# Optimization experiments

Measured on AMD Instinct MI355X. Metric: run time of the kernel, lower is better.

Reference implementation:

```python
import jax, jax.numpy as jnp
import numpy as np

# Loihi neuron / simulation constants (params['neuron'], params['simulation'])
VTH_MANT = 80
V_DECAY = 128
I_DECAY = 1024
REF_DELAY = 1
WGT_EXP = 0
TAU_RHO = 1.0
SCALE_RHO = 1.0
TS = 1
THETA = float(VTH_MANT * (1 << 6))      # 5120, Loihi threshold in fixed-point units
W_SCALE = float(1 << (6 + WGT_EXP))     # 64, weight scaling into Loihi fixed point


def st_floor(x):
    """floor with straight-through gradient (Loihi integer truncation)."""
    return x + jax.lax.stop_gradient(jnp.floor(x) - x)


@jax.custom_vjp
def spike_fn(v):
    # binary spike scaled by 1/Ts, as in SLAYER-Loihi
    return (v >= THETA).astype(v.dtype) * (1.0 / TS)

def _spike_fwd(v):
    return spike_fn(v), v

def _spike_bwd(v, g):
    # SLAYER surrogate: scaleRho/(tauRho*theta) * exp(-|v - theta| / (tauRho*theta))
    pdf = (SCALE_RHO / (TAU_RHO * THETA)) * jnp.exp(-jnp.abs(v - THETA) / (TAU_RHO * THETA))
    return (g * pdf,)

spike_fn.defvjp(_spike_fwd, _spike_bwd)


def quantize_w(w, step=2.0):
    """SLAYER snn.utils.quantize(w, 2) with straight-through gradient."""
    return w + jax.lax.stop_gradient(jnp.round(w / step) * step - w)


def loihi_spikes(wsp):
    """Loihi CUBA neuron scan. wsp: [T, B, C] weighted spike input -> [T, B, C] spikes."""
    i_mul = (4096.0 - I_DECAY) / 4096.0
    v_mul = (4096.0 - V_DECAY) / 4096.0

    def step(carry, x):
        I, V, ref = carry
        I = st_floor(I * i_mul) + W_SCALE * x
        V = st_floor(V * v_mul) + I
        V = jnp.where(ref > 0, jnp.zeros_like(V), V)   # refractory hold at 0
        s = spike_fn(V)
        V = V * (1.0 - s * TS)                          # reset to 0 on spike
        ref = jnp.where(s > 0, REF_DELAY - 1, jnp.maximum(ref - 1, 0))
        return (I, V, ref), s

    B, C = wsp.shape[1], wsp.shape[2]
    init = (jnp.zeros((B, C), wsp.dtype),
            jnp.zeros((B, C), wsp.dtype),
            jnp.zeros((B, C), jnp.int32))
    _, s = jax.lax.scan(step, init, wsp)
    return s


def delay_shift(x):
    """delayShift(x, 1): shift spikes one step forward in time. x: [T, B, C]."""
    return jnp.concatenate([jnp.zeros_like(x[:1]), x[:-1]], axis=0)


def setup_inputs() -> dict:
    key = jax.random.key(0)
    k1, k2, k3 = jax.random.split(key, 3)
    B, IN, HID, OUT, T = 32, 1024, 2048, 512, 256
    spike_input = (jax.random.uniform(k1, (B, IN, T)) < 0.05).astype(jnp.float32)
    W1 = jax.random.normal(k2, (HID, IN), jnp.float32) * 8.0
    W2 = jax.random.normal(k3, (OUT, HID), jnp.float32) * 8.0
    return {"spike_input": spike_input, "W1": W1, "W2": W2}


def reference(spike_input, W1, W2):
    # spike_input: [B, IN, T] binary spikes
    x = jnp.transpose(spike_input, (2, 0, 1))          # [T, B, IN]
    w1 = quantize_w(W1)
    w2 = quantize_w(W2)
    h = jnp.einsum('tbi,hi->tbh', x, w1)               # fc1 per timestep
    s1 = delay_shift(loihi_spikes(h))                  # spikeLoihi + delayShift(1)
    o = jnp.einsum('tbh,oh->tbo', s1, w2)              # fc2 per timestep
    s2 = delay_shift(loihi_spikes(o))
    return jnp.transpose(s2, (1, 2, 0))                # [B, OUT, T]
```

## Files before the change

kernel.cpp:

```cpp
#include <hip/hip_runtime.h>

typedef unsigned char u8;
typedef signed char i8;
typedef unsigned int u32;
typedef __attribute__((ext_vector_type(4))) int i32x4;

#define AS1 __attribute__((address_space(1)))
#define AS3 __attribute__((address_space(3)))

__device__ __forceinline__ void gload_lds16(const void* g, void* l) {
    __builtin_amdgcn_global_load_lds((const AS1 void*)g, (AS3 void*)l, 16, 0, 0);
}

__global__ void transpose_x_bt(const float* __restrict__ X, i8* __restrict__ Xb,
                               int B, int IN, int T) {
    __shared__ float tile[128][33];
    const int t0 = blockIdx.x * 32, i0 = blockIdx.y * 128, b = blockIdx.z;
    const int tx = threadIdx.x & 31, ty = threadIdx.x >> 5;
    const float* src = X + (size_t)b * IN * T;
#pragma unroll
    for (int r = 0; r < 16; ++r) {
        int i = ty + r * 8;
        tile[i][tx] = src[(size_t)(i0 + i) * T + t0 + tx];
    }
    __syncthreads();
    const int cx = threadIdx.x & 31;
    const int tl0 = threadIdx.x >> 5;
#pragma unroll
    for (int r = 0; r < 4; ++r) {
        int tl = tl0 + r * 8;
        uchar4 pk;
        pk.x = (tile[cx * 4 + 0][tl] != 0.f) ? 1 : 0;
        pk.y = (tile[cx * 4 + 1][tl] != 0.f) ? 1 : 0;
        pk.z = (tile[cx * 4 + 2][tl] != 0.f) ? 1 : 0;
        pk.w = (tile[cx * 4 + 3][tl] != 0.f) ? 1 : 0;
        *(uchar4*)&Xb[((size_t)b * T + t0 + tl) * IN + i0 + cx * 4] = pk;
    }
}

__global__ void quant_both(const float4* __restrict__ W1, const float4* __restrict__ W2,
                           char4* __restrict__ W1q, char4* __restrict__ W2q,
                           int n1v, int n2v) {
    int i = blockIdx.x * 256 + threadIdx.x;
    if (i < n1v) {
        float4 w = W1[i];
        char4 q;
        q.x = (i8)(int)rintf(w.x * 0.5f);
        q.y = (i8)(int)rintf(w.y * 0.5f);
        q.z = (i8)(int)rintf(w.z * 0.5f);
        q.w = (i8)(int)rintf(w.w * 0.5f);
        W1q[i] = q;
    } else if (i < n1v + n2v) {
        int j = i - n1v;
        float4 w = W2[j];
        char4 q;
        q.x = (i8)(int)rintf(w.x * 0.5f);
        q.y = (i8)(int)rintf(w.y * 0.5f);
        q.z = (i8)(int)rintf(w.z * 0.5f);
        q.w = (i8)(int)rintf(w.w * 0.5f);
        W2q[j] = q;
    }
}

__global__ __launch_bounds__(256, 4) void gemm1_scan1(
        const i8* __restrict__ A, const i8* __restrict__ Bt,
        i8* __restrict__ S1, int K) {
    __shared__ __align__(16) i8 lds[40960];
    i8*    lA   = lds;
    i8*    lB   = lds + 32768;
    short* hT   = (short*)lds;
    u32*   bits = (u32*)(lds + 32768);

    const int nwg = gridDim.x;
    const int cpx = nwg >> 3;
    const int wg  = (blockIdx.x & 7) * cpx + (blockIdx.x >> 3);
    const int scanw = (blockIdx.x >> 3) & 3;
    const int bx = wg & 31;
    const int by = wg >> 5;
    const int n0 = bx * 64;
    const int m0 = by * 256;

    const int tid  = threadIdx.x;
    const int lane = tid & 63;
    const int w    = tid >> 6;
    const int l15 = lane & 15;
    const int l4  = lane >> 4;
    const int sw  = l15 & 7;

    i32x4 acc[4][4] = {};
    const int flatT = tid * 16;

    for (int k0 = 0; k0 < K; k0 += 128) {
        __syncthreads();
#pragma unroll
        for (int q = 0; q < 8; ++q) {
            int fl = q * 4096 + flatT;
            int r  = fl >> 7;
            int sc = ((fl >> 4) & 7) ^ (r & 7);
            gload_lds16(A + (size_t)(m0 + r) * K + k0 + sc * 16, &lA[fl]);
        }
#pragma unroll
        for (int q = 0; q < 2; ++q) {
            int fl = q * 4096 + flatT;
            int r  = fl >> 7;
            int sc = ((fl >> 4) & 7) ^ (r & 7);
            gload_lds16(Bt + (size_t)(n0 + r) * K + k0 + sc * 16, &lB[fl]);
        }
        __syncthreads();
#pragma unroll
        for (int kk = 0; kk < 2; ++kk) {
            i32x4 af[4], bf[4];
#pragma unroll
            for (int mf = 0; mf < 4; ++mf)
                af[mf] = *(const i32x4*)&lA[(w * 64 + mf * 16 + l15) * 128 +
                                            ((kk * 4 + l4) ^ sw) * 16];
#pragma unroll
            for (int nf = 0; nf < 4; ++nf)
                bf[nf] = *(const i32x4*)&lB[(nf * 16 + l15) * 128 +
                                            ((kk * 4 + l4) ^ sw) * 16];
#pragma unroll
            for (int mf = 0; mf < 4; ++mf)
#pragma unroll
                for (int nf = 0; nf < 4; ++nf)
                    acc[mf][nf] = __builtin_amdgcn_mfma_i32_16x16x64_i8(
                        af[mf], bf[nf], acc[mf][nf], 0, 0, 0);
        }
    }
    __syncthreads();

#pragma unroll
    for (int mf = 0; mf < 4; ++mf)
#pragma unroll
        for (int nf = 0; nf < 4; ++nf) {
            int n = nf * 16 + l15;
            int c = w * 16 + mf * 4 + l4;
            int h0 = acc[mf][nf][0] * 2, h1 = acc[mf][nf][1] * 2;
            int h2 = acc[mf][nf][2] * 2, h3 = acc[mf][nf][3] * 2;
            int2 pk;
            pk.x = (h0 & 0xffff) | (h1 << 16);
            pk.y = (h2 & 0xffff) | (h3 << 16);
            *(int2*)((char*)hT + n * 512 + ((c ^ (n & 15)) << 3)) = pk;
        }
    __syncthreads();

    if (w == scanw) {
        const int n = lane;
        const int nx = n & 15;
        const char* hrow = (char*)hT + n * 512;
        int2 ra[4], rb[4];
#pragma unroll
        for (int q = 0; q < 4; ++q)
            ra[q] = *(const int2*)(hrow + ((q ^ nx) << 3));
        u32 bw[8] = {0, 0, 0, 0, 0, 0, 0, 0};
        float I = 0.f, V = 0.f;
#pragma unroll
        for (int p = 0; p < 16; ++p) {
            if (p < 15) {
#pragma unroll
                for (int q = 0; q < 4; ++q) {
                    int2 v = *(const int2*)(hrow + ((((p + 1) * 4 + q) ^ nx) << 3));
                    if (p & 1) ra[q] = v; else rb[q] = v;
                }
            }
#pragma unroll
            for (int q = 0; q < 4; ++q) {
                int2 hh = (p & 1) ? rb[q] : ra[q];
#pragma unroll
                for (int j = 0; j < 4; ++j) {
                    int t = p * 16 + q * 4 + j;
                    short hv = (j == 0) ? (short)hh.x
                             : (j == 1) ? (short)(hh.x >> 16)
                             : (j == 2) ? (short)hh.y
                                        : (short)(hh.y >> 16);
                    I = floorf(I * 0.75f) + 64.f * (float)hv;
                    V = floorf(V * 0.96875f) + I;
                    if (V >= 5120.f) { bw[t >> 5] |= (1u << (t & 31)); V = 0.f; }
                }
            }
        }
#pragma unroll
        for (int wi = 0; wi < 8; ++wi) bits[wi * 64 + n] = bw[wi];
    }
    __syncthreads();

#pragma unroll
    for (int rep = 0; rep < 16; ++rep) {
        int d   = rep * 256 + tid;
        int tt  = d >> 4;
        int ndq = d & 15;
        u32 outw = 0;
        if (tt > 0) {
            int tb = tt - 1, wi = tb >> 5, sh = tb & 31;
            outw =  ((bits[wi * 64 + ndq * 4 + 0] >> sh) & 1)
                 | (((bits[wi * 64 + ndq * 4 + 1] >> sh) & 1) << 8)
                 | (((bits[wi * 64 + ndq * 4 + 2] >> sh) & 1) << 16)
                 | (((bits[wi * 64 + ndq * 4 + 3] >> sh) & 1) << 24);
        }
        *(u32*)&S1[(size_t)(m0 + tt) * 2048 + n0 + ndq * 4] = outw;
    }
}

__global__ __launch_bounds__(1024, 1) void gemm2_scan2(
        const i8* __restrict__ A, const i8* __restrict__ Bt,
        float* __restrict__ out, int K) {
    __shared__ __align__(16) i8 lds[83968];
    float* hT   = (float*)lds;
    u32*   bits = (u32*)(lds + 81920);

    const int nwg = gridDim.x;
    const int cpx = nwg >> 3;
    const int wg  = (blockIdx.x & 7) * cpx + (blockIdx.x >> 3);
    const int scanw = (blockIdx.x >> 3) & 15;
    const int ox = wg & 7;
    const int by = wg >> 3;
    const int n0 = ox * 64;
    const int m0 = by * 256;

    const int tid  = threadIdx.x;
    const int lane = tid & 63;
    const int w    = tid >> 6;
    const int l15 = lane & 15;
    const int l4  = lane >> 4;
    const int sw  = l15 & 7;

    i32x4 acc[4] = {};
    const int flatT = tid * 16;

    auto STAGE = [&](int buf, int k0) {
        i8* lA = lds + buf * 40960;
        i8* lB = lA + 32768;
#pragma unroll
        for (int q = 0; q < 2; ++q) {
            int fl = q * 16384 + flatT;
            int r  = fl >> 7;
            int sc = ((fl >> 4) & 7) ^ (r & 7);
            gload_lds16(A + (size_t)(m0 + r) * K + k0 + sc * 16, &lA[fl]);
        }
        if (tid < 512) {
            int fl = flatT;
            int r  = fl >> 7;
            int sc = ((fl >> 4) & 7) ^ (r & 7);
            gload_lds16(Bt + (size_t)(n0 + r) * K + k0 + sc * 16, &lB[fl]);
        }
    };

    auto COMPUTE = [&](int buf) {
        const i8* lA = lds + buf * 40960;
        const i8* lB = lA + 32768;
#pragma unroll
        for (int kk = 0; kk < 2; ++kk) {
            i32x4 af, bf[4];
            af = *(const i32x4*)&lA[(w * 16 + l15) * 128 + ((kk * 4 + l4) ^ sw) * 16];
#pragma unroll
            for (int nf = 0; nf < 4; ++nf)
                bf[nf] = *(const i32x4*)&lB[(nf * 16 + l15) * 128 +
                                            ((kk * 4 + l4) ^ sw) * 16];
#pragma unroll
            for (int nf = 0; nf < 4; ++nf)
                acc[nf] = __builtin_amdgcn_mfma_i32_16x16x64_i8(
                    af, bf[nf], acc[nf], 0, 0, 0);
        }
    };

    STAGE(0, 0);
    __syncthreads();
    int cur = 0;
    for (int k0 = 0; k0 < K; k0 += 128) {
        if (k0 + 128 < K) STAGE(cur ^ 1, k0 + 128);
        COMPUTE(cur);
        __syncthreads();
        cur ^= 1;
    }

#pragma unroll
    for (int nf = 0; nf < 4; ++nf) {
        int n = nf * 16 + l15;
        int c = w * 4 + l4;
        float4 pk;
        pk.x = (float)(acc[nf][0] * 2);
        pk.y = (float)(acc[nf][1] * 2);
        pk.z = (float)(acc[nf][2] * 2);
        pk.w = (float)(acc[nf][3] * 2);
        *(float4*)((char*)hT + n * 1024 + ((c ^ (n & 15)) << 4)) = pk;
    }
    __syncthreads();

    if (w == scanw) {
        const int n = lane;
        const int nx = n & 15;
        const char* hrow = (char*)hT + n * 1024;
        float4 ra[4], rb[4];
#pragma unroll
        for (int q = 0; q < 4; ++q)
            ra[q] = *(const float4*)(hrow + ((q ^ nx) << 4));
        u32 bw[8] = {0, 0, 0, 0, 0, 0, 0, 0};
        float I = 0.f, V = 0.f;
#pragma unroll
        for (int p = 0; p < 16; ++p) {
            if (p < 15) {
#pragma unroll
                for (int q = 0; q < 4; ++q) {
                    float4 v = *(const float4*)(hrow + ((((p + 1) * 4 + q) ^ nx) << 4));
                    if (p & 1) ra[q] = v; else rb[q] = v;
                }
            }
#pragma unroll
            for (int q = 0; q < 4; ++q) {
                float4 hh = (p & 1) ? rb[q] : ra[q];
#pragma unroll
                for (int j = 0; j < 4; ++j) {
                    int t = p * 16 + q * 4 + j;
                    float hv = (j == 0) ? hh.x : (j == 1) ? hh.y
                             : (j == 2) ? hh.z : hh.w;
                    I = floorf(I * 0.75f) + 64.f * hv;
                    V = floorf(V * 0.96875f) + I;
                    if (V >= 5120.f) { bw[t >> 5] |= (1u << (t & 31)); V = 0.f; }
                }
            }
        }
#pragma unroll
        for (int wi = 0; wi < 8; ++wi) bits[wi * 64 + n] = bw[wi];
    }
    __syncthreads();

#pragma unroll
    for (int rep = 0; rep < 4; ++rep) {
        int flat = rep * 1024 + tid;
        int o  = flat >> 6;
        int t4 = flat & 63;
        float4 v;
#pragma unroll
        for (int j = 0; j < 4; ++j) {
            int tt = t4 * 4 + j;
            float s = 0.f;
            if (tt > 0) {
                int tb = tt - 1;
                s = (float)((bits[(tb >> 5) * 64 + o] >> (tb & 31)) & 1);
            }
            if (j == 0) v.x = s; else if (j == 1) v.y = s;
            else if (j == 2) v.z = s; else v.w = s;
        }
        *(float4*)&out[((size_t)by * 512 + n0 + o) * 256 + t4 * 4] = v;
    }
}

extern "C" void kernel_launch(void* const* d_in, const int* in_sizes, int n_in,
                              void* d_out, int out_size, void* d_ws, size_t ws_size,
                              hipStream_t stream) {
    const int B = 32, IN = 1024, HID = 2048, OUT = 512, T = 256;
    const float* spikes = (const float*)d_in[0];
    const float* W1 = (const float*)d_in[1];
    const float* W2 = (const float*)d_in[2];
    float* out = (float*)d_out;

    char* ws = (char*)d_ws;
    size_t off = 0;
    auto alloc = [&](size_t bytes) -> void* {
        void* p = ws + off;
        off += (bytes + 255) & ~(size_t)255;
        return p;
    };
    i8* Xb  = (i8*)alloc((size_t)B * T * IN);
    i8* W1q = (i8*)alloc((size_t)HID * IN);
    i8* W2q = (i8*)alloc((size_t)OUT * HID);
    i8* S1  = (i8*)alloc((size_t)B * T * HID);

    transpose_x_bt<<<dim3(T / 32, IN / 128, B), dim3(256), 0, stream>>>(spikes, Xb, B, IN, T);
    {
        int n1v = HID * IN / 4, n2v = OUT * HID / 4;
        quant_both<<<dim3((n1v + n2v + 255) / 256), dim3(256), 0, stream>>>(
            (const float4*)W1, (const float4*)W2, (char4*)W1q, (char4*)W2q, n1v, n2v);
    }
    gemm1_scan1<<<dim3(1024), dim3(256), 0, stream>>>(Xb, W1q, S1, IN);
    gemm2_scan2<<<dim3(256), dim3(1024), 0, stream>>>(S1, W2q, out, HID);
}
```

Measured before the change: 68.13 us.

## Double-buffer gemm1 LDS staging with K-step 64 and adjusted swizzle

Rewrites the gemm1_scan1 main loop as a two-stage LDS double buffer: the next K=64 slice is fetched with global_load_lds into the alternate buffer while MFMAs run on the current one. This removes one barrier per iteration and lets global loads overlap with compute. The K tile shrinks from 128 to 64, so the XOR swizzle is changed to fit 64-byte rows. The trade-off is twice as many loop iterations, each with fewer MFMAs to hide load latency, plus a new bank-conflict pattern from the narrower rows.

```diff
diff --git a/kernel.cpp b/kernel.cpp
--- a/kernel.cpp
+++ b/kernel.cpp
@@ -66,8 +66,6 @@
         const i8* __restrict__ A, const i8* __restrict__ Bt,
         i8* __restrict__ S1, int K) {
     __shared__ __align__(16) i8 lds[40960];
-    i8*    lA   = lds;
-    i8*    lB   = lds + 32768;
     short* hT   = (short*)lds;
     u32*   bits = (u32*)(lds + 32768);
 
@@ -85,48 +83,57 @@
     const int w    = tid >> 6;
     const int l15 = lane & 15;
     const int l4  = lane >> 4;
-    const int sw  = l15 & 7;
+    const int sw  = (l15 >> 1) & 3;
 
     i32x4 acc[4][4] = {};
     const int flatT = tid * 16;
 
-    for (int k0 = 0; k0 < K; k0 += 128) {
+    auto STAGE = [&](int buf, int k0) {
+        i8* lA = lds + buf * 20480;
+        i8* lB = lA + 16384;
+#pragma unroll
+        for (int q = 0; q < 4; ++q) {
+            int fl = q * 4096 + flatT;
+            int r  = fl >> 6;
+            int sc = ((fl >> 4) & 3) ^ ((r >> 1) & 3);
+            gload_lds16(A + (size_t)(m0 + r) * K + k0 + sc * 16, &lA[fl]);
+        }
+        {
+            int fl = flatT;
+            int r  = fl >> 6;
+            int sc = ((fl >> 4) & 3) ^ ((r >> 1) & 3);
+            gload_lds16(Bt + (size_t)(n0 + r) * K + k0 + sc * 16, &lB[fl]);
+        }
+    };
+
+    auto COMPUTE = [&](int buf) {
+        const i8* lA = lds + buf * 20480;
+        const i8* lB = lA + 16384;
+        i32x4 af[4], bf[4];
+#pragma unroll
+        for (int mf = 0; mf < 4; ++mf)
+            af[mf] = *(const i32x4*)&lA[(w * 64 + mf * 16 + l15) * 64 +
+                                        ((l4 ^ sw) << 4)];
+#pragma unroll
+        for (int nf = 0; nf < 4; ++nf)
+            bf[nf] = *(const i32x4*)&lB[(nf * 16 + l15) * 64 + ((l4 ^ sw) << 4)];
+#pragma unroll
+        for (int mf = 0; mf < 4; ++mf)
+#pragma unroll
+            for (int nf = 0; nf < 4; ++nf)
+                acc[mf][nf] = __builtin_amdgcn_mfma_i32_16x16x64_i8(
+                    af[mf], bf[nf], acc[mf][nf], 0, 0, 0);
+    };
+
+    STAGE(0, 0);
+    __syncthreads();
+    int cur = 0;
+    for (int k0 = 0; k0 < K; k0 += 64) {
+        if (k0 + 64 < K) STAGE(cur ^ 1, k0 + 64);
+        COMPUTE(cur);
         __syncthreads();
-#pragma unroll
-        for (int q = 0; q < 8; ++q) {
-            int fl = q * 4096 + flatT;
-            int r  = fl >> 7;
-            int sc = ((fl >> 4) & 7) ^ (r & 7);
-            gload_lds16(A + (size_t)(m0 + r) * K + k0 + sc * 16, &lA[fl]);
-        }
-#pragma unroll
-        for (int q = 0; q < 2; ++q) {
-            int fl = q * 4096 + flatT;
-            int r  = fl >> 7;
-            int sc = ((fl >> 4) & 7) ^ (r & 7);
-            gload_lds16(Bt + (size_t)(n0 + r) * K + k0 + sc * 16, &lB[fl]);
-        }
-        __syncthreads();
-#pragma unroll
-        for (int kk = 0; kk < 2; ++kk) {
-            i32x4 af[4], bf[4];
-#pragma unroll
-            for (int mf = 0; mf < 4; ++mf)
-                af[mf] = *(const i32x4*)&lA[(w * 64 + mf * 16 + l15) * 128 +
-                                            ((kk * 4 + l4) ^ sw) * 16];
-#pragma unroll
-            for (int nf = 0; nf < 4; ++nf)
-                bf[nf] = *(const i32x4*)&lB[(nf * 16 + l15) * 128 +
-                                            ((kk * 4 + l4) ^ sw) * 16];
-#pragma unroll
-            for (int mf = 0; mf < 4; ++mf)
-#pragma unroll
-                for (int nf = 0; nf < 4; ++nf)
-                    acc[mf][nf] = __builtin_amdgcn_mfma_i32_16x16x64_i8(
-                        af[mf], bf[nf], acc[mf][nf], 0, 0, 0);
-        }
-    }
-    __syncthreads();
+        cur ^= 1;
+    }
 
 #pragma unroll
     for (int mf = 0; mf < 4; ++mf)
```

Result: slower. 74.41 us (+9.2%).

## Stage full weight tile in LDS once and stream A fragments directly from global

Applied to the files above, without the earlier changes.

Both GEMM+scan kernels now load the whole B (weight) slice for the block into LDS up front with a new XOR swizzle. A-operand fragments are read straight from global memory into registers and software-prefetched one step ahead, which removes the per-k-step LDS staging and barriers. The K loops are fully unrolled with a fixed trip count, which hardcodes K (1024 and 2048). The larger LDS footprint lowers gemm1 occupancy from 4 to 2 blocks per CU, and gemm2 now needs 128KB of LDS.

```diff
diff --git a/kernel.cpp b/kernel.cpp
--- a/kernel.cpp
+++ b/kernel.cpp
@@ -62,12 +62,10 @@
     }
 }
 
-__global__ __launch_bounds__(256, 4) void gemm1_scan1(
+__global__ __launch_bounds__(256, 2) void gemm1_scan1(
         const i8* __restrict__ A, const i8* __restrict__ Bt,
         i8* __restrict__ S1, int K) {
-    __shared__ __align__(16) i8 lds[40960];
-    i8*    lA   = lds;
-    i8*    lB   = lds + 32768;
+    __shared__ __align__(16) i8 lds[65536];
     short* hT   = (short*)lds;
     u32*   bits = (u32*)(lds + 32768);
 
@@ -85,45 +83,74 @@
     const int w    = tid >> 6;
     const int l15 = lane & 15;
     const int l4  = lane >> 4;
-    const int sw  = l15 & 7;
+
+#pragma unroll
+    for (int q = 0; q < 16; ++q) {
+        int fl = q * 4096 + tid * 16;
+        int r  = fl >> 10;
+        int c  = (fl >> 4) & 63;
+        int sc = c ^ (r & 15);
+        gload_lds16(Bt + (size_t)(n0 + r) * K + sc * 16, &lds[fl]);
+    }
+
+    const i8* pA[4];
+#pragma unroll
+    for (int mf = 0; mf < 4; ++mf)
+        pA[mf] = A + (size_t)(m0 + w * 64 + mf * 16 + l15) * K + l4 * 16;
+
+    i32x4 afA[4], afB[4];
+#pragma unroll
+    for (int mf = 0; mf < 4; ++mf) afA[mf] = *(const i32x4*)(pA[mf]);
+#pragma unroll
+    for (int mf = 0; mf < 4; ++mf) afB[mf] = *(const i32x4*)(pA[mf] + 64);
+
+    __syncthreads();
 
     i32x4 acc[4][4] = {};
-    const int flatT = tid * 16;
-
-    for (int k0 = 0; k0 < K; k0 += 128) {
-        __syncthreads();
-#pragma unroll
-        for (int q = 0; q < 8; ++q) {
-            int fl = q * 4096 + flatT;
-            int r  = fl >> 7;
-            int sc = ((fl >> 4) & 7) ^ (r & 7);
-            gload_lds16(A + (size_t)(m0 + r) * K + k0 + sc * 16, &lA[fl]);
-        }
-#pragma unroll
-        for (int q = 0; q < 2; ++q) {
-            int fl = q * 4096 + flatT;
-            int r  = fl >> 7;
-            int sc = ((fl >> 4) & 7) ^ (r & 7);
-            gload_lds16(Bt + (size_t)(n0 + r) * K + k0 + sc * 16, &lB[fl]);
-        }
-        __syncthreads();
-#pragma unroll
-        for (int kk = 0; kk < 2; ++kk) {
-            i32x4 af[4], bf[4];
-#pragma unroll
-            for (int mf = 0; mf < 4; ++mf)
-                af[mf] = *(const i32x4*)&lA[(w * 64 + mf * 16 + l15) * 128 +
-                                            ((kk * 4 + l4) ^ sw) * 16];
-#pragma unroll
-            for (int nf = 0; nf < 4; ++nf)
-                bf[nf] = *(const i32x4*)&lB[(nf * 16 + l15) * 128 +
-                                            ((kk * 4 + l4) ^ sw) * 16];
+
+#pragma unroll
+    for (int it = 0; it < 8; ++it) {
+        {
+            const int k0 = it * 128;
+            i32x4 bf[4];
+#pragma unroll
+            for (int nf = 0; nf < 4; ++nf) {
+                int n  = nf * 16 + l15;
+                int kc = (k0 >> 4) + l4;
+                bf[nf] = *(const i32x4*)&lds[n * 1024 + ((kc ^ l15) << 4)];
+            }
 #pragma unroll
             for (int mf = 0; mf < 4; ++mf)
 #pragma unroll
                 for (int nf = 0; nf < 4; ++nf)
                     acc[mf][nf] = __builtin_amdgcn_mfma_i32_16x16x64_i8(
-                        af[mf], bf[nf], acc[mf][nf], 0, 0, 0);
+                        afA[mf], bf[nf], acc[mf][nf], 0, 0, 0);
+            if (it < 7) {
+#pragma unroll
+                for (int mf = 0; mf < 4; ++mf)
+                    afA[mf] = *(const i32x4*)(pA[mf] + k0 + 128);
+            }
+        }
+        {
+            const int k0 = it * 128 + 64;
+            i32x4 bf[4];
+#pragma unroll
+            for (int nf = 0; nf < 4; ++nf) {
+                int n  = nf * 16 + l15;
+                int kc = (k0 >> 4) + l4;
+                bf[nf] = *(const i32x4*)&lds[n * 1024 + ((kc ^ l15) << 4)];
+            }
+#pragma unroll
+            for (int mf = 0; mf < 4; ++mf)
+#pragma unroll
+                for (int nf = 0; nf < 4; ++nf)
+                    acc[mf][nf] = __builtin_amdgcn_mfma_i32_16x16x64_i8(
+                        afB[mf], bf[nf], acc[mf][nf], 0, 0, 0);
+            if (it < 7) {
+#pragma unroll
+                for (int mf = 0; mf < 4; ++mf)
+                    afB[mf] = *(const i32x4*)(pA[mf] + k0 + 128);
+            }
         }
     }
     __syncthreads();
@@ -203,9 +230,9 @@
 __global__ __launch_bounds__(1024, 1) void gemm2_scan2(
         const i8* __restrict__ A, const i8* __restrict__ Bt,
         float* __restrict__ out, int K) {
-    __shared__ __align__(16) i8 lds[83968];
+    __shared__ __align__(16) i8 lds[131072];
     float* hT   = (float*)lds;
-    u32*   bits = (u32*)(lds + 81920);
+    u32*   bits = (u32*)(lds + 65536);
 
     const int nwg = gridDim.x;
     const int cpx = nwg >> 3;
@@ -221,56 +248,51 @@
     const int w    = tid >> 6;
     const int l15 = lane & 15;
     const int l4  = lane >> 4;
-    const int sw  = l15 & 7;
+
+#pragma unroll
+    for (int q = 0; q < 8; ++q) {
+        int fl = q * 16384 + tid * 16;
+        int r  = fl >> 11;
+        int c  = (fl >> 4) & 127;
+        int sc = c ^ (r & 15);
+        gload_lds16(Bt + (size_t)(n0 + r) * K + sc * 16, &lds[fl]);
+    }
+
+    const i8* pA = A + (size_t)(m0 + w * 16 + l15) * K + l4 * 16;
+    i32x4 af0 = *(const i32x4*)(pA);
+    i32x4 af1 = *(const i32x4*)(pA + 64);
+    i32x4 af2 = *(const i32x4*)(pA + 128);
+    i32x4 af3 = *(const i32x4*)(pA + 192);
+
+    __syncthreads();
 
     i32x4 acc[4] = {};
-    const int flatT = tid * 16;
-
-    auto STAGE = [&](int buf, int k0) {
-        i8* lA = lds + buf * 40960;
-        i8* lB = lA + 32768;
-#pragma unroll
-        for (int q = 0; q < 2; ++q) {
-            int fl = q * 16384 + flatT;
-            int r  = fl >> 7;
-            int sc = ((fl >> 4) & 7) ^ (r & 7);
-            gload_lds16(A + (size_t)(m0 + r) * K + k0 + sc * 16, &lA[fl]);
-        }
-        if (tid < 512) {
-            int fl = flatT;
-            int r  = fl >> 7;
-            int sc = ((fl >> 4) & 7) ^ (r & 7);
-            gload_lds16(Bt + (size_t)(n0 + r) * K + k0 + sc * 16, &lB[fl]);
-        }
-    };
-
-    auto COMPUTE = [&](int buf) {
-        const i8* lA = lds + buf * 40960;
-        const i8* lB = lA + 32768;
-#pragma unroll
-        for (int kk = 0; kk < 2; ++kk) {
-            i32x4 af, bf[4];
-            af = *(const i32x4*)&lA[(w * 16 + l15) * 128 + ((kk * 4 + l4) ^ sw) * 16];
-#pragma unroll
-            for (int nf = 0; nf < 4; ++nf)
-                bf[nf] = *(const i32x4*)&lB[(nf * 16 + l15) * 128 +
-                                            ((kk * 4 + l4) ^ sw) * 16];
-#pragma unroll
-            for (int nf = 0; nf < 4; ++nf)
-                acc[nf] = __builtin_amdgcn_mfma_i32_16x16x64_i8(
-                    af, bf[nf], acc[nf], 0, 0, 0);
-        }
-    };
-
-    STAGE(0, 0);
-    __syncthreads();
-    int cur = 0;
-    for (int k0 = 0; k0 < K; k0 += 128) {
-        if (k0 + 128 < K) STAGE(cur ^ 1, k0 + 128);
-        COMPUTE(cur);
-        __syncthreads();
-        cur ^= 1;
-    }
+
+#define G2_COMP(AF, K0)                                                        \
+    {                                                                          \
+        i32x4 bf[4];                                                           \
+        _Pragma("unroll")                                                      \
+        for (int nf = 0; nf < 4; ++nf) {                                       \
+            int n  = nf * 16 + l15;                                            \
+            int kc = ((K0) >> 4) + l4;                                         \
+            bf[nf] = *(const i32x4*)&lds[n * 2048 + ((kc ^ l15) << 4)];        \
+        }                                                                      \
+        _Pragma("unroll")                                                      \
+        for (int nf = 0; nf < 4; ++nf)                                         \
+            acc[nf] = __builtin_amdgcn_mfma_i32_16x16x64_i8(                   \
+                AF, bf[nf], acc[nf], 0, 0, 0);                                 \
+    }
+
+#pragma unroll
+    for (int it = 0; it < 8; ++it) {
+        const int kb = it * 256;
+        G2_COMP(af0, kb);       if (it < 7) af0 = *(const i32x4*)(pA + kb + 256);
+        G2_COMP(af1, kb + 64);  if (it < 7) af1 = *(const i32x4*)(pA + kb + 320);
+        G2_COMP(af2, kb + 128); if (it < 7) af2 = *(const i32x4*)(pA + kb + 384);
+        G2_COMP(af3, kb + 192); if (it < 7) af3 = *(const i32x4*)(pA + kb + 448);
+    }
+#undef G2_COMP
+    __syncthreads();
 
 #pragma unroll
     for (int nf = 0; nf < 4; ++nf) {
```

New measurement: 89.10 us. 1.31x slower.
